# Kernel tuning notes

Measured on AMD Instinct MI355X. Metric: run time of the kernel, lower is better.

## Reference

```python
import jax, jax.numpy as jnp
import numpy as np

P_LEN, Q_LEN, BATCH, D, H = 300, 50, 32, 256, 256


def _make_params(key):
    ks = jax.random.split(key, 6)
    s = lambda k, shape, fan: jax.random.normal(k, shape, jnp.float32) * (1.0 / np.sqrt(fan))
    return dict(
        Wq=s(ks[0], (2, H, D), D), bq=jnp.zeros((2, H), jnp.float32),
        Wp=s(ks[1], (2, H, D), D), bp=jnp.zeros((2, H), jnp.float32),
        Wr=s(ks[2], (2, H, H), H), br=jnp.zeros((2, H), jnp.float32),
        Wg=s(ks[3], (2, H), H), bg=jnp.zeros((2,), jnp.float32),
        ln_g=jnp.ones((2, 2 * D), jnp.float32), ln_b=jnp.zeros((2, 2 * D), jnp.float32),
        W_ih=s(ks[4], (2, 4 * H, 2 * D), 2 * D), W_hh=s(ks[5], (2, 4 * H, H), H),
        b_ih=jnp.zeros((2, 4 * H), jnp.float32), b_hh=jnp.zeros((2, 4 * H), jnp.float32),
    )


def setup_inputs() -> dict:
    key = jax.random.key(0)
    k1, k2, k3, k4, kp = jax.random.split(key, 5)
    content_vec = jax.random.normal(k1, (P_LEN, BATCH, D), jnp.float32)
    question_vec = jax.random.normal(k2, (Q_LEN, BATCH, D), jnp.float32)
    p_len = jax.random.randint(k3, (BATCH,), P_LEN // 2, P_LEN + 1)
    q_len = jax.random.randint(k4, (BATCH,), Q_LEN // 2, Q_LEN + 1)
    content_mask = (jnp.arange(P_LEN)[None, :] < p_len[:, None]).astype(jnp.int32)
    question_mask = (jnp.arange(Q_LEN)[None, :] < q_len[:, None]).astype(jnp.int32)
    inp = dict(content_vec=content_vec, content_mask=content_mask,
               question_vec=question_vec, question_mask=question_mask)
    inp.update(_make_params(kp))
    return inp


def _masked_flip(v, mask):
    # v: (P, B, D); mask: (B, P). Reverses the valid prefix of each sequence,
    # leaving padding positions in place (standard Match-LSTM masked_flip).
    P = v.shape[0]
    lengths = mask.sum(axis=1)  # (B,)
    t = jnp.arange(P)[:, None]  # (P, 1)
    idx = jnp.where(t < lengths[None, :], lengths[None, :] - 1 - t, t)  # (P, B)
    idx = jnp.broadcast_to(idx[:, :, None], v.shape)
    return jnp.take_along_axis(v, idx, axis=0)


def _uni_match(cv, qv, qmask, Wq, bq, Wp, bp, Wr, br, Wg, bg, ln_g, ln_b, W_ih, W_hh, b_ih, b_hh):
    # cv: (P, B, D), qv: (Q, B, D), qmask: (B, Q)
    B = cv.shape[1]
    Hh = Wr.shape[0]
    wh = jnp.einsum('qbd,hd->qbh', qv, Wq) + bq      # (Q, B, H), precomputed once
    hp_all = jnp.einsum('pbd,hd->pbh', cv, Wp) + bp  # (P, B, H), precomputed
    pad = (qmask == 0)                               # (B, Q)

    def step(carry, xs):
        h, c = carry
        cv_t, hp_t = xs
        hr = h @ Wr.T + br                                    # (B, H)
        g = jnp.tanh(wh + hp_t[None] + hr[None])              # (Q, B, H)
        alpha = (jnp.einsum('qbh,h->qb', g, Wg) + bg).T       # (B, Q)
        alpha = jax.nn.softmax(jnp.where(pad, -jnp.inf, alpha), axis=1)
        h_alpha = jnp.einsum('bq,qbd->bd', alpha, qv)         # (B, D)
        z = jnp.concatenate([cv_t, h_alpha], axis=1)          # (B, 2D)
        mu = jnp.mean(z, axis=-1, keepdims=True)
        var = jnp.mean((z - mu) ** 2, axis=-1, keepdims=True)
        z = (z - mu) * jax.lax.rsqrt(var + 1e-5) * ln_g + ln_b
        gates = z @ W_ih.T + b_ih + h @ W_hh.T + b_hh         # (B, 4H)
        i_, f_, g_, o_ = jnp.split(gates, 4, axis=1)          # torch LSTMCell order i,f,g,o
        c_n = jax.nn.sigmoid(f_) * c + jax.nn.sigmoid(i_) * jnp.tanh(g_)
        h_n = jax.nn.sigmoid(o_) * jnp.tanh(c_n)
        return (h_n, c_n), h_n

    h0 = jnp.zeros((B, Hh), cv.dtype)
    _, hs = jax.lax.scan(step, (h0, h0), (cv, hp_all))
    return hs  # (P, B, H)


def reference(content_vec, content_mask, question_vec, question_mask,
              Wq, bq, Wp, bp, Wr, br, Wg, bg, ln_g, ln_b, W_ih, W_hh, b_ih, b_hh):
    # Dropout with p=0 (inference) is identity.
    args = lambda i: (Wq[i], bq[i], Wp[i], bp[i], Wr[i], br[i], Wg[i], bg[i],
                      ln_g[i], ln_b[i], W_ih[i], W_hh[i], b_ih[i], b_hh[i])
    right = _uni_match(content_vec, question_vec, question_mask, *args(0))
    cv_flip = _masked_flip(content_vec, content_mask)
    left = _uni_match(cv_flip, question_vec, question_mask, *args(1))
    left = _masked_flip(left, content_mask)
    res = jnp.concatenate([right, left], axis=2)            # (P, B, 2H)
    return content_mask.T[:, :, None].astype(res.dtype) * res
```

## Files before the change

kernel.cpp:

```cpp
#include <hip/hip_runtime.h>
#include <hip/hip_fp16.h>

typedef unsigned int u32;
typedef unsigned long long u64;
typedef _Float16 half2_t __attribute__((ext_vector_type(2)));

static constexpr int PL = 300;
static constexpr int QL = 50;
static constexpr int B  = 32;
static constexpr int D  = 256;
static constexpr int H  = 256;

__device__ __forceinline__ float fdot2(u32 w, u32 x, float acc) {
    return __builtin_amdgcn_fdot2(__builtin_bit_cast(half2_t, w),
                                  __builtin_bit_cast(half2_t, x), acc, false);
}
__device__ __forceinline__ u32 packh2(float a, float b) {
    half2_t h2; h2[0] = (_Float16)a; h2[1] = (_Float16)b;
    return __builtin_bit_cast(u32, h2);
}

__global__ __launch_bounds__(256) void pack_whh(const float* __restrict__ Whh,
                                                u32* __restrict__ dst) {
    int id = blockIdx.x * 256 + threadIdx.x;
    int dd = id >> 17;
    int r  = id & 131071;
    int kc = r >> 12;
    int R  = (r >> 2) & 1023;
    int w  = r & 3;
    int k  = kc * 8 + w * 2;
    const float* s = &Whh[((size_t)dd * 1024 + R) * 256 + k];
    dst[id] = packh2(s[0], s[1]);
}

__global__ __launch_bounds__(256) void pack_wr8(const float* __restrict__ W,
                                                u32* __restrict__ dst) {
    int id = blockIdx.x * 256 + threadIdx.x;
    int g  = id >> 15;
    int r  = id & 32767;
    int kc = r >> 10;
    int c  = (r >> 2) & 255;
    int w  = r & 3;
    int k  = kc * 8 + w * 2;
    const float* s = &W[(g * 256 + c) * 256 + k];
    dst[id] = packh2(s[0], s[1]);
}

__global__ __launch_bounds__(256) void prep_proj(const float* __restrict__ X,
                                                 const float* __restrict__ W,
                                                 const float* __restrict__ Bv,
                                                 __half* __restrict__ out,
                                                 int T, int nt) {
    int id = blockIdx.x;
    int tb = id % nt; id /= nt;
    int b  = id % B;  id /= B;
    int g  = id;
    int t0 = tb * 8;
    int nr = T - t0; if (nr > 8) nr = 8;
    __shared__ __align__(16) float xs[8][256];
    int tid = threadIdx.x;
    for (int r = 0; r < nr; r++) xs[r][tid] = X[((t0 + r) * B + b) * D + tid];
    __syncthreads();
    const float4* wrow = (const float4*)&W[(g * H + tid) * D];
    float bb = Bv[g * H + tid];
    float acc[8];
#pragma unroll
    for (int r = 0; r < 8; r++) acc[r] = bb;
    for (int d4 = 0; d4 < D / 4; d4++) {
        float4 w = wrow[d4];
#pragma unroll
        for (int r = 0; r < 8; r++) {
            float4 x = *(const float4*)&xs[r][d4 * 4];
            acc[r] = fmaf(w.x, x.x, fmaf(w.y, x.y, fmaf(w.z, x.z, fmaf(w.w, x.w, acc[r]))));
        }
    }
    for (int r = 0; r < nr; r++)
        out[((g * B + b) * T + t0 + r) * H + tid] = __float2half(acc[r]);
}

__global__ __launch_bounds__(256) void p1_prep(const float* __restrict__ cv,
                                               const float* __restrict__ Wih,
                                               const float* __restrict__ lng,
                                               __half* __restrict__ P1) {
    int id = blockIdx.x;
    int tb = id % 38; id /= 38;
    int b  = id % 32; id /= 32;
    int dd = id;
    int t0 = tb * 8;
    int nr = PL - t0; if (nr > 8) nr = 8;
    __shared__ __align__(16) float xs[8][256];
    int tid = threadIdx.x;
    float g = lng[dd * 512 + tid];
    for (int r = 0; r < nr; r++)
        xs[r][tid] = cv[((size_t)(t0 + r) * B + b) * D + tid] * g;
    __syncthreads();
    for (int gc = 0; gc < 4; gc++) {
        int R = gc * 256 + tid;
        const float4* wrow = (const float4*)&Wih[((size_t)dd * 1024 + R) * 512];
        float acc[8] = {};
        for (int d4 = 0; d4 < 64; d4++) {
            float4 w = wrow[d4];
#pragma unroll
            for (int r = 0; r < 8; r++) {
                float4 x = *(const float4*)&xs[r][d4 * 4];
                acc[r] = fmaf(w.x, x.x, fmaf(w.y, x.y, fmaf(w.z, x.z, fmaf(w.w, x.w, acc[r]))));
            }
        }
        for (int r = 0; r < nr; r++)
            P1[((size_t)(dd * 32 + b) * PL + t0 + r) * 1024 + R] = __float2half(acc[r]);
    }
}

__global__ __launch_bounds__(256) void vp_prep(const float* __restrict__ qv,
                                               const float* __restrict__ Wih,
                                               const float* __restrict__ lng,
                                               __half* __restrict__ VP) {
    int blk = blockIdx.x;
    int dd = blk >> 8, b = (blk >> 3) & 31, rc = blk & 7;
    __shared__ __align__(16) u32 qg[50 * 128];
    __shared__ __align__(16) u32 wch[128 * 128];
    int tid = threadIdx.x;
    for (int v = tid; v < 6400; v += 256) {
        int q = v >> 7, i = v & 127;
        float a = qv[((size_t)q * 32 + b) * 256 + 2 * i]     * lng[dd * 512 + 256 + 2 * i];
        float c = qv[((size_t)q * 32 + b) * 256 + 2 * i + 1] * lng[dd * 512 + 256 + 2 * i + 1];
        qg[v] = packh2(a, c);
    }
    for (int v = tid; v < 16384; v += 256) {
        int rl = v >> 7, i = v & 127;
        int r = rc * 128 + rl;
        float a = Wih[((size_t)dd * 1024 + r) * 512 + 256 + 2 * i];
        float c = Wih[((size_t)dd * 1024 + r) * 512 + 256 + 2 * i + 1];
        wch[v] = packh2(a, c);
    }
    __syncthreads();
    for (int p = tid; p < 128 * 56; p += 256) {
        int rl = p / 56, q = p % 56;
        int r = rc * 128 + rl;
        float acc = 0.f;
        if (q < 50) {
            const u32* qr = qg + q * 128;
            const u32* wr = wch + rl * 128;
#pragma unroll 8
            for (int i = 0; i < 128; i++) acc = fdot2(wr[i], qr[i], acc);
        }
        VP[((size_t)(dd * 32 + b) * 1024 + r) * 56 + q] = __float2half(acc);
    }
}

__global__ __launch_bounds__(256) void gram_prep(const float* __restrict__ qv,
                                                 float* __restrict__ G,
                                                 float* __restrict__ qs) {
    int b = blockIdx.x;
    __shared__ float qvs[50 * 256];
    int tid = threadIdx.x;
    for (int v = tid; v < 12800; v += 256) {
        int q = v >> 8, k = v & 255;
        qvs[v] = qv[((size_t)q * 32 + b) * 256 + k];
    }
    __syncthreads();
    for (int p = tid; p < 2500; p += 256) {
        int q = p / 50, q2 = p % 50;
        float acc = 0.f;
        for (int k = 0; k < 256; k++) acc = fmaf(qvs[q * 256 + k], qvs[q2 * 256 + k], acc);
        G[((size_t)b * 50 + q) * 50 + q2] = acc;
    }
    if (tid < 52) {
        float s = 0.f;
        if (tid < 50) for (int k = 0; k < 256; k++) s += qvs[tid * 256 + k];
        qs[b * 52 + tid] = s;
    }
}

__global__ __launch_bounds__(256) void cvstats_prep(const float* __restrict__ cv,
                                                    float* __restrict__ st) {
    int blk = blockIdx.x;
    int t = blk >> 5, b = blk & 31;
    int tid = threadIdx.x;
    float v = cv[((size_t)t * 32 + b) * 256 + tid];
    float s = v, s2 = v * v;
#pragma unroll
    for (int m = 32; m; m >>= 1) { s += __shfl_xor(s, m, 64); s2 += __shfl_xor(s2, m, 64); }
    __shared__ float red[8];
    if ((tid & 63) == 0) { red[(tid >> 6) * 2] = s; red[(tid >> 6) * 2 + 1] = s2; }
    __syncthreads();
    if (tid == 0) {
        float S = red[0] + red[2] + red[4] + red[6];
        float S2 = red[1] + red[3] + red[5] + red[7];
        st[((size_t)b * 300 + t) * 2] = S;
        st[((size_t)b * 300 + t) * 2 + 1] = S2;
    }
}

__global__ __launch_bounds__(256) void c1c2_prep(const float* __restrict__ Wih,
                                                 const float* __restrict__ lng,
                                                 const float* __restrict__ lnb,
                                                 const float* __restrict__ bih,
                                                 const float* __restrict__ bhh,
                                                 float* __restrict__ C12) {
    int id = blockIdx.x * 256 + threadIdx.x;
    int dd = id >> 10, R = id & 1023;
    float s1 = 0.f, s2 = 0.f;
    const float* wr = &Wih[((size_t)dd * 1024 + R) * 512];
    for (int k = 0; k < 512; k++) {
        float w = wr[k];
        s1 = fmaf(w, lng[dd * 512 + k], s1);
        s2 = fmaf(w, lnb[dd * 512 + k], s2);
    }
    C12[(size_t)id * 2] = s1;
    C12[(size_t)id * 2 + 1] = s2 + bih[dd * 1024 + R] + bhh[dd * 1024 + R];
}

__global__ __launch_bounds__(256, 1) void scan12(
    const int*   __restrict__ cmask,
    const int*   __restrict__ qmask,
    const float* __restrict__ Wgv,
    const float* __restrict__ bgv,
    const float* __restrict__ brp,
    const u32*   __restrict__ WhhP,
    const u32*   __restrict__ WrP,
    const __half* __restrict__ whp,
    const __half* __restrict__ hpp,
    const __half* __restrict__ P1,
    const __half* __restrict__ VP,
    const float* __restrict__ C12,
    const float* __restrict__ G,
    const float* __restrict__ qsr,
    const float* __restrict__ cvst,
    float* __restrict__ out)
{
    int blk = blockIdx.x;
    int dd = blk >> 5, j = blk & 31;
    int tid = threadIdx.x;
    int lane = tid & 63, wave = tid >> 6;

    __shared__ __align__(16) u32 sh_wh[6400];
    __shared__ float sh_G[50 * 50];
    __shared__ __align__(16) u32 sh_h[128];
    __shared__ float sh_a[256];
    __shared__ float sh_af[64];
    __shared__ __align__(16) u32 sh_al2[28];
    __shared__ float sh_alpha[64];
    __shared__ float sh_qb[64];
    __shared__ float sh_qs[52];
    __shared__ float sh_r2[4];
    __shared__ float sh_cs[2];
    __shared__ int   sh_len1;

    {
        const u32* whsrc = (const u32*)(whp + (size_t)(dd * 32 + j) * QL * H);
        for (int i = tid; i < 6400; i += 256) sh_wh[i] = whsrc[i];
    }
    for (int v = tid; v < 2500; v += 256) sh_G[v] = G[(size_t)j * 2500 + v];
    if (tid < 52) sh_qs[tid] = qsr[j * 52 + tid];
    if (tid < 64) sh_qb[tid] = (tid < QL) ? (qmask[j * QL + tid] ? 0.f : -1e30f) : -1e30f;
    if (tid < 128) sh_h[tid] = 0;
    if (tid == 0) sh_len1 = 0;
    __syncthreads();
    {
        int s = 0;
        for (int tt = tid; tt < PL; tt += 256) s += cmask[j * PL + tt];
#pragma unroll
        for (int m = 32; m; m >>= 1) s += __shfl_xor(s, m, 64);
        if (lane == 0) atomicAdd(&sh_len1, s);
    }
    __syncthreads();
    int len_j = sh_len1;

    float wgr[4];
#pragma unroll
    for (int i = 0; i < 4; i++) wgr[i] = Wgv[dd * H + lane + 64 * i];
    float bgs = bgv[dd];
    float brv = brp[dd * H + tid];
    float C1r[4], C2r[4];
#pragma unroll
    for (int k = 0; k < 4; k++) {
        C1r[k] = C12[((size_t)dd * 1024 + k * 256 + tid) * 2];
        C2r[k] = C12[((size_t)dd * 1024 + k * 256 + tid) * 2 + 1];
    }
    float c_reg = 0.f;

    for (int t = len_j; t < PL; t++)
        out[((size_t)t * B + j) * 512 + dd * 256 + tid] = 0.f;

    const __half* hpb = hpp + (size_t)(dd * 32 + j) * PL * H;
    const u32* VPu = (const u32*)VP;
    const uint4* whq = (const uint4*)WhhP + (size_t)dd * 32 * 1024;
    const uint4* wrq = (const uint4*)WrP  + (size_t)dd * 32 * 256;

    for (int t = 0; t < len_j; t++) {
        int tsj = dd ? (len_j - 1 - t) : t;
        __syncthreads();

        float p1v[4];
#pragma unroll
        for (int k = 0; k < 4; k++)
            p1v[k] = __half2float(P1[((size_t)(dd * 32 + j) * PL + tsj) * 1024 + k * 256 + tid]);
        float hpv = __half2float(hpb[(size_t)tsj * H + tid]);
        if (tid == 0) {
            sh_cs[0] = cvst[((size_t)j * 300 + tsj) * 2];
            sh_cs[1] = cvst[((size_t)j * 300 + tsj) * 2 + 1];
        }

        float g0 = 0.f, g1 = 0.f, g2 = 0.f, g3 = 0.f, hr = 0.f;
#pragma unroll 4
        for (int kc = 0; kc < 32; kc++) {
            uint4 hx = *(const uint4*)(sh_h + kc * 4);
            uint4 wa = whq[kc * 1024 + tid];
            uint4 wb = whq[kc * 1024 + 256 + tid];
            uint4 wc = whq[kc * 1024 + 512 + tid];
            uint4 wd = whq[kc * 1024 + 768 + tid];
            uint4 wr = wrq[kc * 256 + tid];
            g0 = fdot2(wa.x, hx.x, g0); g0 = fdot2(wa.y, hx.y, g0);
            g0 = fdot2(wa.z, hx.z, g0); g0 = fdot2(wa.w, hx.w, g0);
            g1 = fdot2(wb.x, hx.x, g1); g1 = fdot2(wb.y, hx.y, g1);
            g1 = fdot2(wb.z, hx.z, g1); g1 = fdot2(wb.w, hx.w, g1);
            g2 = fdot2(wc.x, hx.x, g2); g2 = fdot2(wc.y, hx.y, g2);
            g2 = fdot2(wc.z, hx.z, g2); g2 = fdot2(wc.w, hx.w, g2);
            g3 = fdot2(wd.x, hx.x, g3); g3 = fdot2(wd.y, hx.y, g3);
            g3 = fdot2(wd.z, hx.z, g3); g3 = fdot2(wd.w, hx.w, g3);
            hr = fdot2(wr.x, hx.x, hr); hr = fdot2(wr.y, hx.y, hr);
            hr = fdot2(wr.z, hx.z, hr); hr = fdot2(wr.w, hx.w, hr);
        }
        sh_a[tid] = hr + brv + hpv;

        uint4 vp[28];
#pragma unroll
        for (int k = 0; k < 4; k++) {
            const uint4* vr = (const uint4*)(VPu + ((size_t)(dd * 32 + j) * 1024 + k * 256 + tid) * 28);
#pragma unroll
            for (int i = 0; i < 7; i++) vp[k * 7 + i] = vr[i];
        }
        __syncthreads();

        {
            float av[4];
#pragma unroll
            for (int i = 0; i < 4; i++) av[i] = sh_a[lane + 64 * i];
            const __half* wh16 = (const __half*)sh_wh;
            for (int q = wave; q < QL; q += 4) {
                float a = 0.f;
#pragma unroll
                for (int i = 0; i < 4; i++) {
                    float xx = (float)wh16[q * 256 + lane + 64 * i] + av[i];
                    float e = __expf(2.f * xx);
                    a = fmaf(wgr[i], (e - 1.f) / (e + 1.f), a);
                }
#pragma unroll
                for (int m = 32; m; m >>= 1) a += __shfl_xor(a, m, 64);
                if (lane == 0) sh_alpha[q] = a + bgs + sh_qb[q];
            }
        }
        __syncthreads();

        if (wave == 0) {
            float v = (lane < QL) ? sh_alpha[lane] : -1e30f;
            float m = v;
#pragma unroll
            for (int s = 32; s; s >>= 1) m = fmaxf(m, __shfl_xor(m, s, 64));
            float e = (lane < QL) ? __expf(v - m) : 0.f;
            float sum = e;
#pragma unroll
            for (int s = 32; s; s >>= 1) sum += __shfl_xor(sum, s, 64);
            float al = (lane < QL) ? e / sum : 0.f;
            sh_af[lane] = al;
            float alo = __shfl_xor(al, 1, 64);
            if (!(lane & 1) && lane < 56) sh_al2[lane >> 1] = packh2(al, alo);
        }
        __syncthreads();

        if (wave == 0) {
            float gd = 0.f;
            if (lane < QL) {
                const float* Grow = sh_G + lane * 50;
                float aq = sh_af[lane];
                for (int q2 = 0; q2 < QL; q2++) gd = fmaf(Grow[q2], sh_af[q2], gd);
                gd *= aq;
            }
#pragma unroll
            for (int m = 32; m; m >>= 1) gd += __shfl_xor(gd, m, 64);
            if (lane == 0) sh_r2[0] = gd;
        } else if (wave == 1) {
            float s = (lane < QL) ? sh_af[lane] * sh_qs[lane] : 0.f;
#pragma unroll
            for (int m = 32; m; m >>= 1) s += __shfl_xor(s, m, 64);
            if (lane == 0) sh_r2[1] = s;
        }
        __syncthreads();

        float aVP[4];
#pragma unroll
        for (int k = 0; k < 4; k++) {
            float acc = 0.f;
#pragma unroll
            for (int i = 0; i < 7; i++) {
                acc = fdot2(vp[k * 7 + i].x, sh_al2[i * 4 + 0], acc);
                acc = fdot2(vp[k * 7 + i].y, sh_al2[i * 4 + 1], acc);
                acc = fdot2(vp[k * 7 + i].z, sh_al2[i * 4 + 2], acc);
                acc = fdot2(vp[k * 7 + i].w, sh_al2[i * 4 + 3], acc);
            }
            aVP[k] = acc;
        }

        float hv;
        {
            float mu = (sh_cs[0] + sh_r2[1]) * (1.f / 512.f);
            float E2 = (sh_cs[1] + sh_r2[0]) * (1.f / 512.f);
            float rs = rsqrtf(E2 - mu * mu + 1e-5f);
            float gk[4] = { g0, g1, g2, g3 };
#pragma unroll
            for (int k = 0; k < 4; k++)
                gk[k] += rs * (p1v[k] + aVP[k]) - rs * mu * C1r[k] + C2r[k];
            float si = 1.f / (1.f + __expf(-gk[0]));
            float sf = 1.f / (1.f + __expf(-gk[1]));
            float so = 1.f / (1.f + __expf(-gk[3]));
            float eg = __expf(2.f * gk[2]); float tg = (eg - 1.f) / (eg + 1.f);
            float c = sf * c_reg + si * tg;
            float ec = __expf(2.f * c); float tc = (ec - 1.f) / (ec + 1.f);
            hv = so * tc;
            c_reg = c;
            float ho = __shfl_xor(hv, 1, 64);
            if (!(tid & 1)) sh_h[tid >> 1] = packh2(hv, ho);
        }

        out[((size_t)tsj * B + j) * 512 + dd * 256 + tid] = hv;
    }
}

extern "C" void kernel_launch(void* const* d_in, const int* in_sizes, int n_in,
                              void* d_out, int out_size, void* d_ws, size_t ws_size,
                              hipStream_t stream) {
    const float* cv    = (const float*)d_in[0];
    const int*   cmask = (const int*)  d_in[1];
    const float* qv    = (const float*)d_in[2];
    const int*   qmask = (const int*)  d_in[3];
    const float* Wq    = (const float*)d_in[4];
    const float* bq    = (const float*)d_in[5];
    const float* Wp    = (const float*)d_in[6];
    const float* bp    = (const float*)d_in[7];
    const float* Wr    = (const float*)d_in[8];
    const float* br    = (const float*)d_in[9];
    const float* Wg    = (const float*)d_in[10];
    const float* bg    = (const float*)d_in[11];
    const float* ln_g  = (const float*)d_in[12];
    const float* ln_b  = (const float*)d_in[13];
    const float* Wih   = (const float*)d_in[14];
    const float* Whh   = (const float*)d_in[15];
    const float* b_ih  = (const float*)d_in[16];
    const float* b_hh  = (const float*)d_in[17];
    float* out = (float*)d_out;

    uint8_t* ws = (uint8_t*)d_ws;
    u32*    WhhP = (u32*)ws;     ws += (size_t)2 * 32 * 1024 * 4 * 4;
    u32*    WrP  = (u32*)ws;     ws += (size_t)2 * 32 * 256 * 4 * 4;
    __half* VP  = (__half*)ws;   ws += (size_t)2 * 32 * 1024 * 56 * 2;
    __half* whp = (__half*)ws;   ws += (size_t)2 * 32 * 50 * 256 * 2;
    __half* hpp = (__half*)ws;   ws += (size_t)2 * 32 * 300 * 256 * 2;
    __half* P1  = (__half*)ws;   ws += (size_t)2 * 32 * 300 * 1024 * 2;
    float*  C12 = (float*)ws;    ws += (size_t)2 * 1024 * 2 * 4;
    float*  G   = (float*)ws;    ws += (size_t)32 * 50 * 50 * 4;
    float*  qs  = (float*)ws;    ws += (size_t)32 * 52 * 4;
    float*  cvs = (float*)ws;

    hipLaunchKernelGGL(pack_whh, dim3(1024), dim3(256), 0, stream, Whh, WhhP);
    hipLaunchKernelGGL(pack_wr8, dim3(256), dim3(256), 0, stream, Wr, WrP);
    hipLaunchKernelGGL(prep_proj, dim3(2 * 32 * 7), dim3(256), 0, stream,
                       qv, Wq, bq, whp, QL, 7);
    hipLaunchKernelGGL(prep_proj, dim3(2 * 32 * 38), dim3(256), 0, stream,
                       cv, Wp, bp, hpp, PL, 38);
    hipLaunchKernelGGL(p1_prep, dim3(2 * 32 * 38), dim3(256), 0, stream,
                       cv, Wih, ln_g, P1);
    hipLaunchKernelGGL(vp_prep, dim3(512), dim3(256), 0, stream, qv, Wih, ln_g, VP);
    hipLaunchKernelGGL(gram_prep, dim3(32), dim3(256), 0, stream, qv, G, qs);
    hipLaunchKernelGGL(cvstats_prep, dim3(9600), dim3(256), 0, stream, cv, cvs);
    hipLaunchKernelGGL(c1c2_prep, dim3(8), dim3(256), 0, stream,
                       Wih, ln_g, ln_b, b_ih, b_hh, C12);
    hipLaunchKernelGGL(scan12, dim3(64), dim3(256), 0, stream,
                       cmask, qmask, Wg, bg, br, WhhP, WrP, whp, hpp, P1, VP, C12, G, qs, cvs,
                       out);
}
```

Baseline: 4.640 ms.

## Widen recurrent scan blocks to 1024 threads, one gate row per thread

The sequential scan kernel goes from 256 to 1024 threads per block. Each thread now computes a single gate row of the W_hh matvec and the VP attention dot product instead of four, and writes it to shared memory. The first 256 threads then combine the four gates into the LSTM cell update. This cuts the serial per-thread work on the latency-bound recurrence and raises memory-level parallelism. In exchange it adds an extra barrier per step, more shared memory, and synchronisation across 16 waves, of which 12 sit idle during parts of each step.

```diff
diff --git a/kernel.cpp b/kernel.cpp
--- a/kernel.cpp
+++ b/kernel.cpp
@@ -211,7 +211,7 @@
     C12[(size_t)id * 2 + 1] = s2 + bih[dd * 1024 + R] + bhh[dd * 1024 + R];
 }
 
-__global__ __launch_bounds__(256, 1) void scan12(
+__global__ __launch_bounds__(1024, 1) void scan13(
     const int*   __restrict__ cmask,
     const int*   __restrict__ qmask,
     const float* __restrict__ Wgv,
@@ -238,6 +238,7 @@
     __shared__ float sh_G[50 * 50];
     __shared__ __align__(16) u32 sh_h[128];
     __shared__ float sh_a[256];
+    __shared__ float sh_gk[1024];
     __shared__ float sh_af[64];
     __shared__ __align__(16) u32 sh_al2[28];
     __shared__ float sh_alpha[64];
@@ -249,17 +250,20 @@
 
     {
         const u32* whsrc = (const u32*)(whp + (size_t)(dd * 32 + j) * QL * H);
-        for (int i = tid; i < 6400; i += 256) sh_wh[i] = whsrc[i];
-    }
-    for (int v = tid; v < 2500; v += 256) sh_G[v] = G[(size_t)j * 2500 + v];
+        for (int i = tid; i < 6400; i += 1024) sh_wh[i] = whsrc[i];
+    }
+    for (int v = tid; v < 2500; v += 1024) sh_G[v] = G[(size_t)j * 2500 + v];
     if (tid < 52) sh_qs[tid] = qsr[j * 52 + tid];
-    if (tid < 64) sh_qb[tid] = (tid < QL) ? (qmask[j * QL + tid] ? 0.f : -1e30f) : -1e30f;
-    if (tid < 128) sh_h[tid] = 0;
+    if (tid >= 64 && tid < 128) {
+        int q = tid - 64;
+        sh_qb[q] = (q < QL) ? (qmask[j * QL + q] ? 0.f : -1e30f) : -1e30f;
+    }
+    if (tid >= 128 && tid < 256) sh_h[tid - 128] = 0;
     if (tid == 0) sh_len1 = 0;
     __syncthreads();
     {
         int s = 0;
-        for (int tt = tid; tt < PL; tt += 256) s += cmask[j * PL + tt];
+        for (int tt = tid; tt < PL; tt += 1024) s += cmask[j * PL + tt];
 #pragma unroll
         for (int m = 32; m; m >>= 1) s += __shfl_xor(s, m, 64);
         if (lane == 0) atomicAdd(&sh_len1, s);
@@ -271,66 +275,52 @@
 #pragma unroll
     for (int i = 0; i < 4; i++) wgr[i] = Wgv[dd * H + lane + 64 * i];
     float bgs = bgv[dd];
-    float brv = brp[dd * H + tid];
-    float C1r[4], C2r[4];
-#pragma unroll
-    for (int k = 0; k < 4; k++) {
-        C1r[k] = C12[((size_t)dd * 1024 + k * 256 + tid) * 2];
-        C2r[k] = C12[((size_t)dd * 1024 + k * 256 + tid) * 2 + 1];
-    }
+    float brv = (tid < 256) ? brp[dd * H + tid] : 0.f;
+    float C1r = C12[((size_t)dd * 1024 + tid) * 2];
+    float C2r = C12[((size_t)dd * 1024 + tid) * 2 + 1];
     float c_reg = 0.f;
 
-    for (int t = len_j; t < PL; t++)
-        out[((size_t)t * B + j) * 512 + dd * 256 + tid] = 0.f;
+    if (tid < 256)
+        for (int t = len_j; t < PL; t++)
+            out[((size_t)t * B + j) * 512 + dd * 256 + tid] = 0.f;
 
     const __half* hpb = hpp + (size_t)(dd * 32 + j) * PL * H;
     const u32* VPu = (const u32*)VP;
     const uint4* whq = (const uint4*)WhhP + (size_t)dd * 32 * 1024;
     const uint4* wrq = (const uint4*)WrP  + (size_t)dd * 32 * 256;
+    bool ishr = (tid < 256);
 
     for (int t = 0; t < len_j; t++) {
         int tsj = dd ? (len_j - 1 - t) : t;
         __syncthreads();
 
-        float p1v[4];
-#pragma unroll
-        for (int k = 0; k < 4; k++)
-            p1v[k] = __half2float(P1[((size_t)(dd * 32 + j) * PL + tsj) * 1024 + k * 256 + tid]);
-        float hpv = __half2float(hpb[(size_t)tsj * H + tid]);
+        float p1v = __half2float(P1[((size_t)(dd * 32 + j) * PL + tsj) * 1024 + tid]);
+        float hpv = ishr ? __half2float(hpb[(size_t)tsj * H + tid]) : 0.f;
         if (tid == 0) {
             sh_cs[0] = cvst[((size_t)j * 300 + tsj) * 2];
             sh_cs[1] = cvst[((size_t)j * 300 + tsj) * 2 + 1];
         }
-
-        float g0 = 0.f, g1 = 0.f, g2 = 0.f, g3 = 0.f, hr = 0.f;
-#pragma unroll 4
+        uint4 vp[7];
+        {
+            const uint4* vr = (const uint4*)(VPu + ((size_t)(dd * 32 + j) * 1024 + tid) * 28);
+#pragma unroll
+            for (int i = 0; i < 7; i++) vp[i] = vr[i];
+        }
+
+        float g0 = 0.f, hr = 0.f;
+#pragma unroll 8
         for (int kc = 0; kc < 32; kc++) {
             uint4 hx = *(const uint4*)(sh_h + kc * 4);
             uint4 wa = whq[kc * 1024 + tid];
-            uint4 wb = whq[kc * 1024 + 256 + tid];
-            uint4 wc = whq[kc * 1024 + 512 + tid];
-            uint4 wd = whq[kc * 1024 + 768 + tid];
-            uint4 wr = wrq[kc * 256 + tid];
             g0 = fdot2(wa.x, hx.x, g0); g0 = fdot2(wa.y, hx.y, g0);
             g0 = fdot2(wa.z, hx.z, g0); g0 = fdot2(wa.w, hx.w, g0);
-            g1 = fdot2(wb.x, hx.x, g1); g1 = fdot2(wb.y, hx.y, g1);
-            g1 = fdot2(wb.z, hx.z, g1); g1 = fdot2(wb.w, hx.w, g1);
-            g2 = fdot2(wc.x, hx.x, g2); g2 = fdot2(wc.y, hx.y, g2);
-            g2 = fdot2(wc.z, hx.z, g2); g2 = fdot2(wc.w, hx.w, g2);
-            g3 = fdot2(wd.x, hx.x, g3); g3 = fdot2(wd.y, hx.y, g3);
-            g3 = fdot2(wd.z, hx.z, g3); g3 = fdot2(wd.w, hx.w, g3);
-            hr = fdot2(wr.x, hx.x, hr); hr = fdot2(wr.y, hx.y, hr);
-            hr = fdot2(wr.z, hx.z, hr); hr = fdot2(wr.w, hx.w, hr);
-        }
-        sh_a[tid] = hr + brv + hpv;
-
-        uint4 vp[28];
-#pragma unroll
-        for (int k = 0; k < 4; k++) {
-            const uint4* vr = (const uint4*)(VPu + ((size_t)(dd * 32 + j) * 1024 + k * 256 + tid) * 28);
-#pragma unroll
-            for (int i = 0; i < 7; i++) vp[k * 7 + i] = vr[i];
-        }
+            if (ishr) {
+                uint4 wr = wrq[kc * 256 + tid];
+                hr = fdot2(wr.x, hx.x, hr); hr = fdot2(wr.y, hx.y, hr);
+                hr = fdot2(wr.z, hx.z, hr); hr = fdot2(wr.w, hx.w, hr);
+            }
+        }
+        if (ishr) sh_a[tid] = hr + brv + hpv;
         __syncthreads();
 
         {
@@ -338,7 +328,7 @@
 #pragma unroll
             for (int i = 0; i < 4; i++) av[i] = sh_a[lane + 64 * i];
             const __half* wh16 = (const __half*)sh_wh;
-            for (int q = wave; q < QL; q += 4) {
+            for (int q = wave; q < QL; q += 16) {
                 float a = 0.f;
 #pragma unroll
                 for (int i = 0; i < 4; i++) {
@@ -388,42 +378,37 @@
         }
         __syncthreads();
 
-        float aVP[4];
-#pragma unroll
-        for (int k = 0; k < 4; k++) {
+        {
             float acc = 0.f;
 #pragma unroll
             for (int i = 0; i < 7; i++) {
-                acc = fdot2(vp[k * 7 + i].x, sh_al2[i * 4 + 0], acc);
-                acc = fdot2(vp[k * 7 + i].y, sh_al2[i * 4 + 1], acc);
-                acc = fdot2(vp[k * 7 + i].z, sh_al2[i * 4 + 2], acc);
-                acc = fdot2(vp[k * 7 + i].w, sh_al2[i * 4 + 3], acc);
+                acc = fdot2(vp[i].x, sh_al2[i * 4 + 0], acc);
+                acc = fdot2(vp[i].y, sh_al2[i * 4 + 1], acc);
+                acc = fdot2(vp[i].z, sh_al2[i * 4 + 2], acc);
+                acc = fdot2(vp[i].w, sh_al2[i * 4 + 3], acc);
             }
-            aVP[k] = acc;
-        }
-
-        float hv;
-        {
             float mu = (sh_cs[0] + sh_r2[1]) * (1.f / 512.f);
             float E2 = (sh_cs[1] + sh_r2[0]) * (1.f / 512.f);
             float rs = rsqrtf(E2 - mu * mu + 1e-5f);
-            float gk[4] = { g0, g1, g2, g3 };
-#pragma unroll
-            for (int k = 0; k < 4; k++)
-                gk[k] += rs * (p1v[k] + aVP[k]) - rs * mu * C1r[k] + C2r[k];
-            float si = 1.f / (1.f + __expf(-gk[0]));
-            float sf = 1.f / (1.f + __expf(-gk[1]));
-            float so = 1.f / (1.f + __expf(-gk[3]));
-            float eg = __expf(2.f * gk[2]); float tg = (eg - 1.f) / (eg + 1.f);
+            sh_gk[tid] = g0 + rs * (p1v + acc) - rs * mu * C1r + C2r;
+        }
+        __syncthreads();
+
+        if (ishr) {
+            float gi = sh_gk[tid], gf = sh_gk[256 + tid];
+            float gg = sh_gk[512 + tid], go = sh_gk[768 + tid];
+            float si = 1.f / (1.f + __expf(-gi));
+            float sf = 1.f / (1.f + __expf(-gf));
+            float so = 1.f / (1.f + __expf(-go));
+            float eg = __expf(2.f * gg); float tg = (eg - 1.f) / (eg + 1.f);
             float c = sf * c_reg + si * tg;
             float ec = __expf(2.f * c); float tc = (ec - 1.f) / (ec + 1.f);
-            hv = so * tc;
+            float hv = so * tc;
             c_reg = c;
             float ho = __shfl_xor(hv, 1, 64);
             if (!(tid & 1)) sh_h[tid >> 1] = packh2(hv, ho);
-        }
-
-        out[((size_t)tsj * B + j) * 512 + dd * 256 + tid] = hv;
+            out[((size_t)tsj * B + j) * 512 + dd * 256 + tid] = hv;
+        }
     }
 }
 
@@ -475,7 +460,7 @@
     hipLaunchKernelGGL(cvstats_prep, dim3(9600), dim3(256), 0, stream, cv, cvs);
     hipLaunchKernelGGL(c1c2_prep, dim3(8), dim3(256), 0, stream,
                        Wih, ln_g, ln_b, b_ih, b_hh, C12);
-    hipLaunchKernelGGL(scan12, dim3(64), dim3(256), 0, stream,
+    hipLaunchKernelGGL(scan13, dim3(64), dim3(1024), 0, stream,
                        cmask, qmask, Wg, bg, br, WhhP, WrP, whp, hpp, P1, VP, C12, G, qs, cvs,
                        out);
 }
```

Result: faster. 4.142 ms (-10.7%).
